# Kernel optimization log

Hardware: AMD Instinct MI355X
Metric: run time of the kernel (lower is better)

## Reference

```python
import jax, jax.numpy as jnp
import numpy as np

HIDDEN = 512
TEXT_DIM = 768
NUM_HEADS = 8
NUM_GROUPS = 32
GN_EPS = 1e-5
COS_EPS = 1e-6


def setup_inputs() -> dict:
    key = jax.random.key(0)
    ks = jax.random.split(key, 9)
    s = 0.02
    return {
        "x": jax.random.normal(ks[0], (16, HIDDEN, 64, 64), jnp.float32),
        "text_emb": jax.random.normal(ks[1], (16, 77, TEXT_DIM), jnp.float32),
        "gn_weight": jnp.ones((HIDDEN,), jnp.float32),
        "gn_bias": jnp.zeros((HIDDEN,), jnp.float32),
        "Wq": jax.random.normal(ks[2], (HIDDEN, HIDDEN), jnp.float32) * s,
        "Wk": jax.random.normal(ks[3], (HIDDEN, TEXT_DIM), jnp.float32) * s,
        "Wv": jax.random.normal(ks[4], (HIDDEN, TEXT_DIM), jnp.float32) * s,
        "Wo": jax.random.normal(ks[5], (HIDDEN, HIDDEN), jnp.float32) * s,
        "bo": jnp.zeros((HIDDEN,), jnp.float32),
    }


def reference(x, text_emb, gn_weight, gn_bias, Wq, Wk, Wv, Wo, bo):
    B, C, H, W = x.shape
    N_img = H * W
    nh, hd = NUM_HEADS, C // NUM_HEADS

    # GroupNorm(32, C): normalize over (channels-in-group, H, W)
    xg = x.reshape(B, NUM_GROUPS, -1)
    mu = xg.mean(axis=-1, keepdims=True)
    var = jnp.mean(jnp.square(xg - mu), axis=-1, keepdims=True)
    xn = ((xg - mu) * jax.lax.rsqrt(var + GN_EPS)).reshape(B, C, H, W)
    xn = xn * gn_weight[None, :, None, None] + gn_bias[None, :, None, None]

    x_flat = xn.reshape(B, C, N_img).transpose(0, 2, 1)  # [B, N_img, C]

    q = jnp.einsum('bnc,dc->bnd', x_flat, Wq)            # [B, N_img, C]
    k = jnp.einsum('btc,dc->btd', text_emb, Wk)          # [B, N_text, C]
    v = jnp.einsum('btc,dc->btd', text_emb, Wv)

    # split heads -> [B, nh, N, hd]
    q = q.reshape(B, N_img, nh, hd).transpose(0, 2, 1, 3)
    k = k.reshape(B, -1, nh, hd).transpose(0, 2, 1, 3)
    v = v.reshape(B, -1, nh, hd).transpose(0, 2, 1, 3)

    # cosine-sim attention: L2-normalize q and k, scale = 1.0
    q = q / (jnp.linalg.norm(q, axis=-1, keepdims=True) + COS_EPS)
    k = k / (jnp.linalg.norm(k, axis=-1, keepdims=True) + COS_EPS)

    scores = jnp.einsum('bhqd,bhkd->bhqk', q, k)         # [B, nh, N_img, N_text]
    attn = jax.nn.softmax(scores, axis=-1)
    out = jnp.einsum('bhqk,bhkd->bhqd', attn, v)         # [B, nh, N_img, hd]

    out = out.transpose(0, 2, 1, 3).reshape(B, N_img, C)
    out = jnp.einsum('bnc,dc->bnd', out, Wo) + bo
    out = out.transpose(0, 2, 1).reshape(B, C, H, W)
    return x + out
```

## Files before the change

### kernel.cpp

```cpp
#include <hip/hip_runtime.h>
#include <math.h>


typedef unsigned short u16;
typedef __attribute__((ext_vector_type(8))) __bf16 bf16x8;
typedef __attribute__((ext_vector_type(4))) float f32x4;

typedef __attribute__((address_space(1))) unsigned int as1_u32;
typedef __attribute__((address_space(3))) unsigned int as3_u32;

__device__ __forceinline__ float b2f(u16 u) {
  union { unsigned int i; float f; } c; c.i = ((unsigned int)u) << 16; return c.f;
}
__device__ __forceinline__ u16 f2b(float f) {
  union { float f; unsigned int i; } c; c.f = f;
  unsigned int i = c.i + 0x7fffu + ((c.i >> 16) & 1u);
  return (u16)(i >> 16);
}

__device__ __forceinline__ void g2lds16(const void* g, void* l) {
  __builtin_amdgcn_global_load_lds((const as1_u32*)g, (as3_u32*)l, 16, 0, 0);
}

__global__ void k_castall(const float* __restrict__ Wq, const float* __restrict__ Wk,
                          const float* __restrict__ Wv, const float* __restrict__ Wo,
                          const float* __restrict__ text,
                          u16* __restrict__ wq_b, u16* __restrict__ wkv_b,
                          u16* __restrict__ wo_b, u16* __restrict__ text_b) {
  const int i = blockIdx.x * 256 + threadIdx.x, st = gridDim.x * 256;
  for (int j = i; j < 262144; j += st) wq_b[j] = f2b(Wq[j]);
  for (int j = i; j < 393216; j += st) wkv_b[j] = f2b(Wk[j]);
  for (int j = i; j < 393216; j += st) wkv_b[393216 + j] = f2b(Wv[j]);
  for (int j = i; j < 262144; j += st) wo_b[j] = f2b(Wo[j]);
  for (int j = i; j < 946176; j += st) text_b[j] = f2b(text[j]);
}

__global__ __launch_bounds__(256) void k_gnstats(const float* __restrict__ x,
                                                 float* __restrict__ stats) {
  int bg = blockIdx.x;
  const float4* p = (const float4*)(x + (size_t)bg * 65536);
  float s = 0.f, ss = 0.f;
  for (int i = threadIdx.x; i < 16384; i += 256) {
    float4 v = p[i];
    s  += v.x + v.y + v.z + v.w;
    ss += v.x*v.x + v.y*v.y + v.z*v.z + v.w*v.w;
  }
  for (int o = 1; o < 64; o <<= 1) { s += __shfl_xor(s, o, 64); ss += __shfl_xor(ss, o, 64); }
  __shared__ float as_[4], bs_[4];
  int w = threadIdx.x >> 6;
  if ((threadIdx.x & 63) == 0) { as_[w] = s; bs_[w] = ss; }
  __syncthreads();
  if (threadIdx.x == 0) {
    s  = as_[0] + as_[1] + as_[2] + as_[3];
    ss = bs_[0] + bs_[1] + bs_[2] + bs_[3];
    float mu  = s * (1.f / 65536.f);
    float var = ss * (1.f / 65536.f) - mu * mu;
    stats[2*bg]   = mu;
    stats[2*bg+1] = rsqrtf(var + 1e-5f);
  }
}

__global__ __launch_bounds__(256, 2) void k_qproj(
    const float* __restrict__ x, const float* __restrict__ stats,
    const float* __restrict__ gw, const float* __restrict__ gb,
    const u16* __restrict__ Wqb, u16* __restrict__ qb) {
  __shared__ u16 Al[128 * 64];
  __shared__ u16 Bl[256 * 64];
  __shared__ float cw[512], cb[512];
  const int tid = threadIdx.x;
  const int o = blockIdx.x;
  const int mi = ((o >> 4) << 3) + (o & 7);
  const int ni = (o >> 3) & 1;
  const int m0 = mi << 7, n0 = ni << 8;
  const int b = m0 >> 12, hw0 = m0 & 4095;

  for (int c = tid; c < 512; c += 256) {
    const int g = (b << 5) + (c >> 4);
    const float mu = stats[2*g], rs = stats[2*g+1];
    const float wg = gw[c] * rs;
    cw[c] = wg; cb[c] = gb[c] - mu * wg;
  }

  const int l = tid & 63, w = tid >> 6;
  const int wm = (w & 1) << 6;
  const int wn = (w >> 1) << 7;
  const int lr = l & 15, lg = l >> 4;

  f32x4 acc[4][8];
#pragma unroll
  for (int i = 0; i < 4; ++i)
#pragma unroll
    for (int j = 0; j < 8; ++j) acc[i][j] = {0.f, 0.f, 0.f, 0.f};

  const int rl = l >> 3, slot = l & 7;
  const int c8 = (slot ^ rl) << 3;
  int brow[8];
#pragma unroll
  for (int j = 0; j < 8; ++j) brow[j] = n0 + (w << 6) + (j << 3) + rl;

  const int tokl = tid & 127;
  const int chg = tid >> 7;
  const float* xb = x + (((size_t)b) << 9) * 4096;
  __syncthreads();

  for (int ks = 0; ks < 8; ++ks) {
#pragma unroll
    for (int j = 0; j < 8; ++j)
      g2lds16(Wqb + (size_t)brow[j] * 512 + (ks << 6) + c8,
              Bl + (((w << 6) + (j << 3)) << 6));
#pragma unroll
    for (int jj = 0; jj < 8; ++jj) {
      const int ch4 = (((chg << 3) + jj) << 2);
      const int c = (ks << 6) + ch4;
      const float v0 = xb[(size_t)(c + 0) * 4096 + hw0 + tokl];
      const float v1 = xb[(size_t)(c + 1) * 4096 + hw0 + tokl];
      const float v2 = xb[(size_t)(c + 2) * 4096 + hw0 + tokl];
      const float v3 = xb[(size_t)(c + 3) * 4096 + hw0 + tokl];
      union { __bf16 h[4]; ushort4 u; } pk;
      pk.h[0] = (__bf16)(v0 * cw[c + 0] + cb[c + 0]);
      pk.h[1] = (__bf16)(v1 * cw[c + 1] + cb[c + 1]);
      pk.h[2] = (__bf16)(v2 * cw[c + 2] + cb[c + 2]);
      pk.h[3] = (__bf16)(v3 * cw[c + 3] + cb[c + 3]);
      const int sl = (((ch4 >> 3) ^ (tokl & 7)) << 3) + (ch4 & 7);
      *(ushort4*)(Al + (tokl << 6) + sl) = pk.u;
    }
    __syncthreads();
    bf16x8 af[4][2];
#pragma unroll
    for (int i = 0; i < 4; ++i) {
      const int ar = wm + i * 16 + lr;
      af[i][0] = *(const bf16x8*)(Al + (ar << 6) + (((lg    ) ^ (ar & 7)) << 3));
      af[i][1] = *(const bf16x8*)(Al + (ar << 6) + (((lg + 4) ^ (ar & 7)) << 3));
    }
#pragma unroll
    for (int j = 0; j < 8; ++j) {
      const int br = wn + j * 16 + lr;
      const bf16x8 b0 = *(const bf16x8*)(Bl + (br << 6) + (((lg    ) ^ (br & 7)) << 3));
      const bf16x8 b1 = *(const bf16x8*)(Bl + (br << 6) + (((lg + 4) ^ (br & 7)) << 3));
#pragma unroll
      for (int i = 0; i < 4; ++i) {
        acc[i][j] = __builtin_amdgcn_mfma_f32_16x16x32_bf16(af[i][0], b0, acc[i][j], 0, 0, 0);
        acc[i][j] = __builtin_amdgcn_mfma_f32_16x16x32_bf16(af[i][1], b1, acc[i][j], 0, 0, 0);
      }
    }
    __syncthreads();
  }

  const int lg4 = lg << 2;
#pragma unroll
  for (int i = 0; i < 4; ++i) {
#pragma unroll
    for (int r = 0; r < 4; ++r) {
      const int row = m0 + wm + i * 16 + lg4 + r;
#pragma unroll
      for (int h2 = 0; h2 < 2; ++h2) {
        float ss = 0.f;
#pragma unroll
        for (int j = h2 * 4; j < h2 * 4 + 4; ++j) {
          const float v = acc[i][j][r]; ss += v * v;
        }
        ss += __shfl_xor(ss, 1, 64); ss += __shfl_xor(ss, 2, 64);
        ss += __shfl_xor(ss, 4, 64); ss += __shfl_xor(ss, 8, 64);
        const float sc = 1.f / (sqrtf(ss) + 1e-6f);
#pragma unroll
        for (int j = h2 * 4; j < h2 * 4 + 4; ++j)
          qb[(size_t)row * 512 + n0 + wn + j * 16 + lr] = f2b(acc[i][j][r] * sc);
      }
    }
  }
}

template <int MODE>
__global__ __launch_bounds__(256) void k_gemm(
    const u16* __restrict__ A, const u16* __restrict__ BT,
    int M, int N, int K,
    float* __restrict__ outf,
    const float* __restrict__ xres, const float* __restrict__ bias) {
  __shared__ u16 Al[128 * 64];
  __shared__ u16 Bl[128 * 64];
  const int tid = threadIdx.x;
  const int l = tid & 63, w = tid >> 6;

  const int nwg = gridDim.x * gridDim.y;
  int lin = blockIdx.y * gridDim.x + blockIdx.x;
  lin = (lin & 7) * (nwg >> 3) + (lin >> 3);
  const int m0 = (lin / gridDim.x) << 7, n0 = (lin % gridDim.x) << 7;

  const int wm = (w >> 1) << 6, wn = (w & 1) << 6;
  const int lr = l & 15, lg = l >> 4;

  f32x4 acc[4][4];
#pragma unroll
  for (int i = 0; i < 4; ++i)
#pragma unroll
    for (int j = 0; j < 4; ++j) acc[i][j] = {0.f, 0.f, 0.f, 0.f};

  const int rl = l >> 3, slot = l & 7;
  const int c8 = (slot ^ rl) << 3;
  int arow[4], brow[4];
#pragma unroll
  for (int j = 0; j < 4; ++j) {
    const int r_local = (w << 5) + (j << 3) + rl;
    arow[j] = min(m0 + r_local, M - 1);
    brow[j] = n0 + r_local;
  }

  const int ksteps = K >> 6;
  for (int ks = 0; ks < ksteps; ++ks) {
    const int kb = (ks << 6) + c8;
#pragma unroll
    for (int j = 0; j < 4; ++j)
      g2lds16(A + (size_t)arow[j] * K + kb, Al + (((w << 5) + (j << 3)) << 6));
#pragma unroll
    for (int j = 0; j < 4; ++j)
      g2lds16(BT + (size_t)brow[j] * K + kb, Bl + (((w << 5) + (j << 3)) << 6));
    __syncthreads();
    bf16x8 bfr[4][2];
#pragma unroll
    for (int j = 0; j < 4; ++j) {
      const int br = wn + j * 16 + lr;
      bfr[j][0] = *(const bf16x8*)(Bl + (br << 6) + (((lg    ) ^ (br & 7)) << 3));
      bfr[j][1] = *(const bf16x8*)(Bl + (br << 6) + (((lg + 4) ^ (br & 7)) << 3));
    }
#pragma unroll
    for (int i = 0; i < 4; ++i) {
      const int ar = wm + i * 16 + lr;
      const bf16x8 a0 = *(const bf16x8*)(Al + (ar << 6) + (((lg    ) ^ (ar & 7)) << 3));
      const bf16x8 a1 = *(const bf16x8*)(Al + (ar << 6) + (((lg + 4) ^ (ar & 7)) << 3));
#pragma unroll
      for (int j = 0; j < 4; ++j) {
        acc[i][j] = __builtin_amdgcn_mfma_f32_16x16x32_bf16(a0, bfr[j][0], acc[i][j], 0, 0, 0);
        acc[i][j] = __builtin_amdgcn_mfma_f32_16x16x32_bf16(a1, bfr[j][1], acc[i][j], 0, 0, 0);
      }
    }
    __syncthreads();
  }

  const int lg4 = lg << 2;
#pragma unroll
  for (int i = 0; i < 4; ++i) {
#pragma unroll
    for (int j = 0; j < 4; ++j) {
#pragma unroll
      for (int r = 0; r < 4; ++r) {
        const int row = m0 + wm + i * 16 + lg4 + r;
        const int col = n0 + wn + j * 16 + lr;
        const float v = acc[i][j][r];
        if (MODE == 0) {
          if (row < M) outf[(size_t)row * N + col] = v;
        } else {
          const int bb = col >> 12, hw = col & 4095;
          const size_t oo = (((size_t)bb << 9) + row) * 4096 + hw;
          outf[oo] = xres[oo] + bias[row] + v;
        }
      }
    }
  }
}

__global__ __launch_bounds__(64) void k_kvnorm(const float* __restrict__ kv,
                                               u16* __restrict__ kn,
                                               u16* __restrict__ vn) {
  const int row = blockIdx.x;
  const int h = blockIdx.y;
  const int d = threadIdx.x;
  const int b = row / 77, t = row - b * 77;
  const float kx = kv[(size_t)row * 1024 + h * 64 + d];
  float ss = kx * kx;
  for (int o = 1; o < 64; o <<= 1) ss += __shfl_xor(ss, o, 64);
  const float sc = 1.f / (sqrtf(ss) + 1e-6f);
  const size_t ob = (((size_t)(b * 8 + h)) * 77 + t) * 64 + d;
  kn[ob] = f2b(kx * sc);
  vn[ob] = f2b(kv[(size_t)row * 1024 + 512 + h * 64 + d]);
}

__global__ __launch_bounds__(256) void k_attn2(
    const u16* __restrict__ q, const u16* __restrict__ kn,
    const u16* __restrict__ vn, u16* __restrict__ out) {
  __shared__ u16 Kl[96 * 72];
  __shared__ u16 Vt[64 * 104];
  __shared__ u16 Pl[64 * 104];
  const int qt = blockIdx.x, h = blockIdx.y, b = blockIdx.z;
  const size_t kvb = ((size_t)(b * 8 + h)) * (77 * 64);
  const int tid = threadIdx.x;
  for (int u = tid; u < 768; u += 256) {
    const int row = u >> 3, c8v = (u & 7) << 3;
    uint4 v = make_uint4(0, 0, 0, 0);
    if (row < 77) v = *(const uint4*)(kn + kvb + row * 64 + c8v);
    *(uint4*)(Kl + row * 72 + c8v) = v;
  }
  for (int u = tid; u < 768; u += 256) {
    const int row = u >> 3, c8v = (u & 7) << 3;
    uint4 v = make_uint4(0, 0, 0, 0);
    if (row < 77) v = *(const uint4*)(vn + kvb + row * 64 + c8v);
    const u16* pv = (const u16*)&v;
#pragma unroll
    for (int j = 0; j < 8; ++j) Vt[(c8v + j) * 104 + row] = pv[j];
  }
  __syncthreads();
  const int l = tid & 63, w = tid >> 6;
  const int lr = l & 15, lg = l >> 4;

  const int qrow = (b << 12) + (qt << 6) + (w << 4) + lr;
  bf16x8 af0 = *(const bf16x8*)(q + (size_t)qrow * 512 + h * 64 + lg * 8);
  bf16x8 af1 = *(const bf16x8*)(q + (size_t)qrow * 512 + h * 64 + 32 + lg * 8);
  f32x4 s[6];
#pragma unroll
  for (int nt = 0; nt < 6; ++nt) {
    s[nt] = {0.f, 0.f, 0.f, 0.f};
    bf16x8 bk0 = *(const bf16x8*)(Kl + (nt * 16 + lr) * 72 + lg * 8);
    bf16x8 bk1 = *(const bf16x8*)(Kl + (nt * 16 + lr) * 72 + 32 + lg * 8);
    s[nt] = __builtin_amdgcn_mfma_f32_16x16x32_bf16(af0, bk0, s[nt], 0, 0, 0);
    s[nt] = __builtin_amdgcn_mfma_f32_16x16x32_bf16(af1, bk1, s[nt], 0, 0, 0);
  }
#pragma unroll
  for (int r = 0; r < 4; ++r) {
    if (lr >= 13) s[4][r] = -1e30f;
    s[5][r] = -1e30f;
  }
#pragma unroll
  for (int r = 0; r < 4; ++r) {
    float m = s[0][r];
#pragma unroll
    for (int nt = 1; nt < 6; ++nt) m = fmaxf(m, s[nt][r]);
    m = fmaxf(m, __shfl_xor(m, 1, 64)); m = fmaxf(m, __shfl_xor(m, 2, 64));
    m = fmaxf(m, __shfl_xor(m, 4, 64)); m = fmaxf(m, __shfl_xor(m, 8, 64));
    float sum = 0.f;
#pragma unroll
    for (int nt = 0; nt < 6; ++nt) { s[nt][r] = __expf(s[nt][r] - m); sum += s[nt][r]; }
    sum += __shfl_xor(sum, 1, 64); sum += __shfl_xor(sum, 2, 64);
    sum += __shfl_xor(sum, 4, 64); sum += __shfl_xor(sum, 8, 64);
    const float inv = 1.f / sum;
    const int qlocal = (w << 4) + (lg << 2) + r;
#pragma unroll
    for (int nt = 0; nt < 6; ++nt)
      Pl[qlocal * 104 + nt * 16 + lr] = f2b(s[nt][r] * inv);
  }
  __syncthreads();

  bf16x8 pa0 = *(const bf16x8*)(Pl + ((w << 4) + lr) * 104 + lg * 8);
  bf16x8 pa1 = *(const bf16x8*)(Pl + ((w << 4) + lr) * 104 + 32 + lg * 8);
  bf16x8 pa2 = *(const bf16x8*)(Pl + ((w << 4) + lr) * 104 + 64 + lg * 8);
  f32x4 o[4];
#pragma unroll
  for (int nt = 0; nt < 4; ++nt) {
    o[nt] = {0.f, 0.f, 0.f, 0.f};
    bf16x8 bv0 = *(const bf16x8*)(Vt + (nt * 16 + lr) * 104 + lg * 8);
    bf16x8 bv1 = *(const bf16x8*)(Vt + (nt * 16 + lr) * 104 + 32 + lg * 8);
    bf16x8 bv2 = *(const bf16x8*)(Vt + (nt * 16 + lr) * 104 + 64 + lg * 8);
    o[nt] = __builtin_amdgcn_mfma_f32_16x16x32_bf16(pa0, bv0, o[nt], 0, 0, 0);
    o[nt] = __builtin_amdgcn_mfma_f32_16x16x32_bf16(pa1, bv1, o[nt], 0, 0, 0);
    o[nt] = __builtin_amdgcn_mfma_f32_16x16x32_bf16(pa2, bv2, o[nt], 0, 0, 0);
  }
#pragma unroll
  for (int r = 0; r < 4; ++r) {
    const int n = (b << 12) + (qt << 6) + (w << 4) + (lg << 2) + r;
#pragma unroll
    for (int nt = 0; nt < 4; ++nt)
      out[(size_t)n * 512 + h * 64 + nt * 16 + lr] = f2b(o[nt][r]);
  }
}

extern "C" void kernel_launch(void* const* d_in, const int* in_sizes, int n_in,
                              void* d_out, int out_size, void* d_ws, size_t ws_size,
                              hipStream_t stream) {
  (void)in_sizes; (void)n_in; (void)out_size; (void)ws_size;
  const float* x    = (const float*)d_in[0];
  const float* text = (const float*)d_in[1];
  const float* gnw  = (const float*)d_in[2];
  const float* gnb  = (const float*)d_in[3];
  const float* Wq   = (const float*)d_in[4];
  const float* Wk   = (const float*)d_in[5];
  const float* Wv   = (const float*)d_in[6];
  const float* Wo   = (const float*)d_in[7];
  const float* bo   = (const float*)d_in[8];
  float* out = (float*)d_out;

  char* ws = (char*)d_ws;
  size_t off = 0;
  auto alloc = [&](size_t bytes) -> void* {
    void* p = ws + off; off += (bytes + 255) & ~(size_t)255; return p;
  };
  float* stats = (float*)alloc(512 * 2 * 4);
  u16* wq_b    = (u16*)alloc((size_t)512 * 512 * 2);
  u16* wkv_b   = (u16*)alloc((size_t)1024 * 768 * 2);
  u16* wo_b    = (u16*)alloc((size_t)512 * 512 * 2);
  u16* text_b  = (u16*)alloc((size_t)1232 * 768 * 2);
  float* kv_f  = (float*)alloc((size_t)1232 * 1024 * 4);
  u16* kn      = (u16*)alloc((size_t)16 * 8 * 77 * 64 * 2);
  u16* vn      = (u16*)alloc((size_t)16 * 8 * 77 * 64 * 2);
  u16* ao      = (u16*)alloc((size_t)65536 * 512 * 2);
  u16* qb      = (u16*)alloc((size_t)65536 * 512 * 2);

  k_castall<<<dim3(512), 256, 0, stream>>>(Wq, Wk, Wv, Wo, text,
                                           wq_b, wkv_b, wo_b, text_b);

  k_gnstats<<<dim3(512), 256, 0, stream>>>(x, stats);

  k_gemm<0><<<dim3(8, 10), 256, 0, stream>>>(text_b, wkv_b, 1232, 1024, 768,
                                             kv_f, nullptr, nullptr);
  k_kvnorm<<<dim3(1232, 8), 64, 0, stream>>>(kv_f, kn, vn);

  k_qproj<<<dim3(1024), 256, 0, stream>>>(x, stats, gnw, gnb, wq_b, qb);

  k_attn2<<<dim3(64, 8, 16), 256, 0, stream>>>(qb, kn, vn, ao);

  k_gemm<2><<<dim3(512, 4), 256, 0, stream>>>(wo_b, ao, 512, 65536, 512,
                                              out, x, bo);
}
```

Measured before the change: 297.2 us.

## Fuse KV projection and K-normalization into the Q-projection kernel launch

```diff
diff --git a/kernel.cpp b/kernel.cpp
--- a/kernel.cpp
+++ b/kernel.cpp
@@ -60,14 +60,104 @@
   }
 }
 
-__global__ __launch_bounds__(256, 2) void k_qproj(
+__global__ __launch_bounds__(256, 2) void k_qproj_kv(
     const float* __restrict__ x, const float* __restrict__ stats,
     const float* __restrict__ gw, const float* __restrict__ gb,
-    const u16* __restrict__ Wqb, u16* __restrict__ qb) {
+    const u16* __restrict__ Wqb, u16* __restrict__ qb,
+    const u16* __restrict__ textb, const u16* __restrict__ wkvb,
+    u16* __restrict__ kn, u16* __restrict__ vn) {
   __shared__ u16 Al[128 * 64];
   __shared__ u16 Bl[256 * 64];
   __shared__ float cw[512], cb[512];
   const int tid = threadIdx.x;
+  const int l = tid & 63, w = tid >> 6;
+  const int lr = l & 15, lg = l >> 4;
+  const int lg4 = lg << 2;
+  const int rl = l >> 3, slot = l & 7;
+  const int c8 = (slot ^ rl) << 3;
+
+  if (blockIdx.x >= 1024) {
+    const int kb = blockIdx.x - 1024;
+    const int m0 = (kb >> 3) << 7, n0 = (kb & 7) << 7;
+    const int wm = (w >> 1) << 6, wn = (w & 1) << 6;
+
+    f32x4 acc[4][4];
+#pragma unroll
+    for (int i = 0; i < 4; ++i)
+#pragma unroll
+      for (int j = 0; j < 4; ++j) acc[i][j] = {0.f, 0.f, 0.f, 0.f};
+
+    int arow[4], brow[4];
+#pragma unroll
+    for (int j = 0; j < 4; ++j) {
+      const int r_local = (w << 5) + (j << 3) + rl;
+      arow[j] = min(m0 + r_local, 1231);
+      brow[j] = n0 + r_local;
+    }
+
+    for (int ks = 0; ks < 12; ++ks) {
+      const int kcol = (ks << 6) + c8;
+#pragma unroll
+      for (int j = 0; j < 4; ++j)
+        g2lds16(textb + (size_t)arow[j] * 768 + kcol, Al + (((w << 5) + (j << 3)) << 6));
+#pragma unroll
+      for (int j = 0; j < 4; ++j)
+        g2lds16(wkvb + (size_t)brow[j] * 768 + kcol, Bl + (((w << 5) + (j << 3)) << 6));
+      __syncthreads();
+      bf16x8 bfr[4][2];
+#pragma unroll
+      for (int j = 0; j < 4; ++j) {
+        const int br = wn + j * 16 + lr;
+        bfr[j][0] = *(const bf16x8*)(Bl + (br << 6) + (((lg    ) ^ (br & 7)) << 3));
+        bfr[j][1] = *(const bf16x8*)(Bl + (br << 6) + (((lg + 4) ^ (br & 7)) << 3));
+      }
+#pragma unroll
+      for (int i = 0; i < 4; ++i) {
+        const int ar = wm + i * 16 + lr;
+        const bf16x8 a0 = *(const bf16x8*)(Al + (ar << 6) + (((lg    ) ^ (ar & 7)) << 3));
+        const bf16x8 a1 = *(const bf16x8*)(Al + (ar << 6) + (((lg + 4) ^ (ar & 7)) << 3));
+#pragma unroll
+        for (int j = 0; j < 4; ++j) {
+          acc[i][j] = __builtin_amdgcn_mfma_f32_16x16x32_bf16(a0, bfr[j][0], acc[i][j], 0, 0, 0);
+          acc[i][j] = __builtin_amdgcn_mfma_f32_16x16x32_bf16(a1, bfr[j][1], acc[i][j], 0, 0, 0);
+        }
+      }
+      __syncthreads();
+    }
+
+    const int col0 = n0 + wn;
+#pragma unroll
+    for (int i = 0; i < 4; ++i) {
+#pragma unroll
+      for (int r = 0; r < 4; ++r) {
+        const int row = m0 + wm + i * 16 + lg4 + r;
+        if (row < 1232) {
+          const int bq = row / 77, tq = row - bq * 77;
+          if (col0 < 512) {
+            float ss = 0.f;
+#pragma unroll
+            for (int j = 0; j < 4; ++j) { const float v = acc[i][j][r]; ss += v * v; }
+            ss += __shfl_xor(ss, 1, 64); ss += __shfl_xor(ss, 2, 64);
+            ss += __shfl_xor(ss, 4, 64); ss += __shfl_xor(ss, 8, 64);
+            const float sc = 1.f / (sqrtf(ss) + 1e-6f);
+            const int h = col0 >> 6;
+            const size_t ob = (((size_t)(bq * 8 + h)) * 77 + tq) * 64;
+#pragma unroll
+            for (int j = 0; j < 4; ++j)
+              kn[ob + j * 16 + lr] = f2b(acc[i][j][r] * sc);
+          } else {
+            const int h = (col0 - 512) >> 6;
+            const size_t ob = (((size_t)(bq * 8 + h)) * 77 + tq) * 64;
+#pragma unroll
+            for (int j = 0; j < 4; ++j)
+              vn[ob + j * 16 + lr] = f2b(acc[i][j][r]);
+          }
+        }
+      }
+    }
+    return;
+  }
+
   const int o = blockIdx.x;
   const int mi = ((o >> 4) << 3) + (o & 7);
   const int ni = (o >> 3) & 1;
@@ -81,10 +171,8 @@
     cw[c] = wg; cb[c] = gb[c] - mu * wg;
   }
 
-  const int l = tid & 63, w = tid >> 6;
   const int wm = (w & 1) << 6;
   const int wn = (w >> 1) << 7;
-  const int lr = l & 15, lg = l >> 4;
 
   f32x4 acc[4][8];
 #pragma unroll
@@ -92,8 +180,6 @@
 #pragma unroll
     for (int j = 0; j < 8; ++j) acc[i][j] = {0.f, 0.f, 0.f, 0.f};
 
-  const int rl = l >> 3, slot = l & 7;
-  const int c8 = (slot ^ rl) << 3;
   int brow[8];
 #pragma unroll
   for (int j = 0; j < 8; ++j) brow[j] = n0 + (w << 6) + (j << 3) + rl;
@@ -146,7 +232,6 @@
     __syncthreads();
   }
 
-  const int lg4 = lg << 2;
 #pragma unroll
   for (int i = 0; i < 4; ++i) {
 #pragma unroll
@@ -170,8 +255,7 @@
   }
 }
 
-template <int MODE>
-__global__ __launch_bounds__(256) void k_gemm(
+__global__ __launch_bounds__(256) void k_gemm2(
     const u16* __restrict__ A, const u16* __restrict__ BT,
     int M, int N, int K,
     float* __restrict__ outf,
@@ -245,33 +329,12 @@
       for (int r = 0; r < 4; ++r) {
         const int row = m0 + wm + i * 16 + lg4 + r;
         const int col = n0 + wn + j * 16 + lr;
-        const float v = acc[i][j][r];
-        if (MODE == 0) {
-          if (row < M) outf[(size_t)row * N + col] = v;
-        } else {
-          const int bb = col >> 12, hw = col & 4095;
-          const size_t oo = (((size_t)bb << 9) + row) * 4096 + hw;
-          outf[oo] = xres[oo] + bias[row] + v;
-        }
-      }
-    }
-  }
-}
-
-__global__ __launch_bounds__(64) void k_kvnorm(const float* __restrict__ kv,
-                                               u16* __restrict__ kn,
-                                               u16* __restrict__ vn) {
-  const int row = blockIdx.x;
-  const int h = blockIdx.y;
-  const int d = threadIdx.x;
-  const int b = row / 77, t = row - b * 77;
-  const float kx = kv[(size_t)row * 1024 + h * 64 + d];
-  float ss = kx * kx;
-  for (int o = 1; o < 64; o <<= 1) ss += __shfl_xor(ss, o, 64);
-  const float sc = 1.f / (sqrtf(ss) + 1e-6f);
-  const size_t ob = (((size_t)(b * 8 + h)) * 77 + t) * 64 + d;
-  kn[ob] = f2b(kx * sc);
-  vn[ob] = f2b(kv[(size_t)row * 1024 + 512 + h * 64 + d]);
+        const int bb = col >> 12, hw = col & 4095;
+        const size_t oo = (((size_t)bb << 9) + row) * 4096 + hw;
+        outf[oo] = xres[oo] + bias[row] + acc[i][j][r];
+      }
+    }
+  }
 }
 
 __global__ __launch_bounds__(256) void k_attn2(
@@ -386,7 +449,6 @@
   u16* wkv_b   = (u16*)alloc((size_t)1024 * 768 * 2);
   u16* wo_b    = (u16*)alloc((size_t)512 * 512 * 2);
   u16* text_b  = (u16*)alloc((size_t)1232 * 768 * 2);
-  float* kv_f  = (float*)alloc((size_t)1232 * 1024 * 4);
   u16* kn      = (u16*)alloc((size_t)16 * 8 * 77 * 64 * 2);
   u16* vn      = (u16*)alloc((size_t)16 * 8 * 77 * 64 * 2);
   u16* ao      = (u16*)alloc((size_t)65536 * 512 * 2);
@@ -397,14 +459,11 @@
 
   k_gnstats<<<dim3(512), 256, 0, stream>>>(x, stats);
 
-  k_gemm<0><<<dim3(8, 10), 256, 0, stream>>>(text_b, wkv_b, 1232, 1024, 768,
-                                             kv_f, nullptr, nullptr);
-  k_kvnorm<<<dim3(1232, 8), 64, 0, stream>>>(kv_f, kn, vn);
-
-  k_qproj<<<dim3(1024), 256, 0, stream>>>(x, stats, gnw, gnb, wq_b, qb);
+  k_qproj_kv<<<dim3(1104), 256, 0, stream>>>(x, stats, gnw, gnb, wq_b, qb,
+                                             text_b, wkv_b, kn, vn);
 
   k_attn2<<<dim3(64, 8, 16), 256, 0, stream>>>(qb, kn, vn, ao);
 
-  k_gemm<2><<<dim3(512, 4), 256, 0, stream>>>(wo_b, ao, 512, 65536, 512,
-                                              out, x, bo);
-}
+  k_gemm2<<<dim3(512, 4), 256, 0, stream>>>(wo_b, ao, 512, 65536, 512,
+                                            out, x, bo);
+}
```

Result: faster. 287.3 us (-3.3%).
